# Performance work log

Hardware: AMD Instinct MI355X
Metric: run time of the kernel (lower is better)

## Reference

```python
import jax, jax.numpy as jnp
import numpy as np

N = 20000      # nodes
E = 160000     # edges (before self loops)
F = 256        # num_features
HID = 64       # hidden_channels
H = 4          # num_heads
HC = HID // H  # head channels = 16
C = 10         # num_classes
K = 3          # hops
ALPHA = 0.1
CST = 1e-5


def setup_inputs() -> dict:
    key = jax.random.key(0)
    ks = jax.random.split(key, 12)
    node_feat = jax.random.normal(ks[0], (N, F), dtype=jnp.float32)
    edge_index = jax.random.randint(ks[1], (2, E), 0, N, dtype=jnp.int32)

    def lin(k, fan_in, fan_out):
        b = 1.0 / np.sqrt(fan_in)
        kw, kb = jax.random.split(k)
        W = jax.random.uniform(kw, (fan_in, fan_out), jnp.float32, -b, b)
        bias = jax.random.uniform(kb, (fan_out,), jnp.float32, -b, b)
        return W, bias

    W_in, b_in = lin(ks[2], F, HID)
    Wq, bq = lin(ks[3], HID, H * HC)
    Wk, bk = lin(ks[4], HID, H * HC)
    Wv, bv = lin(ks[5], HID, H * C)
    W_out, b_out = lin(ks[6], H * C, C)

    # hopwise: alpha*(1-alpha)^k, last entry (1-alpha)^K
    hw = ALPHA * (1 - ALPHA) ** np.arange(K + 1, dtype=np.float32)
    hw[-1] = (1 - ALPHA) ** K
    hopwise = jnp.asarray(hw, dtype=jnp.float32)
    # temp: uniform one-head vector normalized by L1, tiled per head
    bound = np.sqrt(3.0 / (K + 1))
    onehead = jax.random.uniform(ks[7], (K + 1,), jnp.float32, -bound, bound)
    onehead = onehead / jnp.sum(jnp.abs(onehead))
    temp = jnp.tile(onehead[None, :], (H, 1))  # [H, K+1]

    return dict(node_feat=node_feat, edge_index=edge_index, W_in=W_in, b_in=b_in,
                Wq=Wq, bq=bq, Wk=Wk, bk=bk, Wv=Wv, bv=bv,
                W_out=W_out, b_out=b_out, hopwise=hopwise, temp=temp)


def reference(node_feat, edge_index, W_in, b_in, Wq, bq, Wk, bk, Wv, bv,
              W_out, b_out, hopwise, temp):
    # add self loops
    loops = jnp.arange(N, dtype=edge_index.dtype)
    ei = jnp.concatenate([edge_index, jnp.stack([loops, loops])], axis=1)
    row, col = ei[0], ei[1]
    # symmetric-normalized laplacian weights
    deg = jnp.zeros((N,), node_feat.dtype).at[col].add(1.0)
    dis = jnp.where(deg > 0, 1.0 / jnp.sqrt(jnp.maximum(deg, 1.0)), 0.0)
    norm = dis[row] * dis[col]  # [E+N]

    x = jax.nn.relu(node_feat @ W_in + b_in)                      # [N, HID]
    Q = (1.0 + jax.nn.elu(x @ Wq + bq)).reshape(N, H, HC)
    Kt = (1.0 + jax.nn.elu(x @ Wk + bk)).reshape(N, H, HC)
    V = (x @ Wv + bv).reshape(N, H, C)

    M = jnp.einsum('nhi,nhj->nhij', Kt, V)                        # [N, H, HC, C]
    hidden = V * hopwise[0]
    # NOTE: faithful to torch: softmax over dim=-2 of temp [H, K+1] == head axis
    layerwise = jax.nn.softmax(temp, axis=0)                      # [H, K+1]

    for hop in range(K):
        M = jax.ops.segment_sum(norm[:, None, None, None] * M[row], col, num_segments=N)
        Kt = jax.ops.segment_sum(norm[:, None, None] * Kt[row], col, num_segments=N)
        Hh = jnp.einsum('nhi,nhij->nhj', Q, M)                    # [N, H, C]
        Cd = jnp.einsum('nhi,nhi->nh', Q, Kt)[..., None] + CST    # [N, H, 1]
        gamma = hopwise[hop + 1] * layerwise[:, hop + 1][:, None]  # [H, 1]
        hidden = hidden + gamma * (Hh / Cd)

    out = hidden.reshape(N, H * C) @ W_out + b_out                # [N, C]
    return out
```

## Files before the change

### kernel.cpp

```cpp
#include <hip/hip_runtime.h>
#include <stdint.h>

#define kN   20000
#define kE   160000
#define kET  (kN + kE)
#define kF   256
#define kHID 64
#define kH   4
#define kHC  16
#define kC   10
#define kK   3
#define kCST 1e-5f
#define kBN  32

__device__ __forceinline__ uint16_t f2bf(float x) {
    uint32_t u = __float_as_uint(x);
    u += 0x7fffu + ((u >> 16) & 1u);
    return (uint16_t)(u >> 16);
}
__device__ __forceinline__ float lo16(uint32_t p) { return __uint_as_float(p << 16); }
__device__ __forceinline__ float hi16(uint32_t p) { return __uint_as_float(p & 0xffff0000u); }
__device__ __forceinline__ uint32_t pack2(float a, float b) {
    return ((uint32_t)f2bf(b) << 16) | (uint32_t)f2bf(a);
}

__global__ void deg_kernel(const int* __restrict__ ei, int* __restrict__ deg) {
    int e = blockIdx.x * blockDim.x + threadIdx.x;
    if (e >= kET) return;
    int c = (e < kE) ? ei[kE + e] : (e - kE);
    atomicAdd(&deg[c], 1);
}

__global__ __launch_bounds__(1024) void scan_kernel(
    const int* __restrict__ deg, int* __restrict__ ptr,
    const float* __restrict__ hopwise, const float* __restrict__ temp,
    float* __restrict__ gammas) {
    __shared__ int wsums[16];
    __shared__ int wexcl[16];
    const int CH = 20;
    int t = threadIdx.x;
    int base = t * CH;
    int s = 0;
    for (int i = 0; i < CH; ++i) {
        int idx = base + i;
        if (idx < kN) s += deg[idx];
    }
    int incl = s;
#pragma unroll
    for (int off = 1; off < 64; off <<= 1) {
        int v = __shfl_up(incl, off, 64);
        if ((t & 63) >= off) incl += v;
    }
    int wid = t >> 6;
    if ((t & 63) == 63) wsums[wid] = incl;
    __syncthreads();
    if (t < 16) {
        int p = 0;
        for (int j = 0; j < t; ++j) p += wsums[j];
        wexcl[t] = p;
    }
    __syncthreads();
    int running = wexcl[wid] + incl - s;
    for (int i = 0; i < CH; ++i) {
        int idx = base + i;
        if (idx < kN) { ptr[idx] = running; running += deg[idx]; }
    }
    if (base < kN && base + CH >= kN) ptr[kN] = running;
    if (t == 0) {
        for (int k = 1; k <= kK; ++k) {
            float mx = -1e30f;
            for (int h = 0; h < kH; ++h) mx = fmaxf(mx, temp[h * (kK + 1) + k]);
            float ex[kH]; float sum = 0.f;
            for (int h = 0; h < kH; ++h) { ex[h] = __expf(temp[h * (kK + 1) + k] - mx); sum += ex[h]; }
            for (int h = 0; h < kH; ++h) gammas[(k - 1) * kH + h] = hopwise[k] * ex[h] / sum;
        }
    }
}

__global__ void scatter_kernel(const int* __restrict__ ei, const int* __restrict__ deg,
                               const int* __restrict__ ptr, int* __restrict__ cursor,
                               int* __restrict__ src, float* __restrict__ wgt) {
    int e = blockIdx.x * blockDim.x + threadIdx.x;
    if (e >= kET) return;
    int r, c;
    if (e < kE) { r = ei[e]; c = ei[kE + e]; } else { r = c = e - kE; }
    float wv = rsqrtf((float)deg[r]) * rsqrtf((float)deg[c]);
    int pos = ptr[c] + atomicAdd(&cursor[c], 1);
    src[pos] = r;
    wgt[pos] = wv;
}

__global__ __launch_bounds__(256) void proj_kernel(
    const float* __restrict__ feat, const float* __restrict__ W_in, const float* __restrict__ b_in,
    const float* __restrict__ Wq, const float* __restrict__ bq,
    const float* __restrict__ Wk, const float* __restrict__ bk,
    const float* __restrict__ Wv, const float* __restrict__ bv,
    const float* __restrict__ hopwise,
    float* __restrict__ Qg, float* __restrict__ Ktg, float* __restrict__ hidden,
    float* __restrict__ Vg) {
    __shared__ float sF[kBN * 68];
    __shared__ float sW[64 * 68];
    __shared__ float sX[kBN * 68];

    int t = threadIdx.x;
    int tx = t & 15, ty = t >> 4;
    int n0 = blockIdx.x * kBN;
    int r0 = ty * 2, r1 = ty * 2 + 1;

    float acc[2][4];
#pragma unroll
    for (int i = 0; i < 2; ++i)
#pragma unroll
        for (int j = 0; j < 4; ++j) acc[i][j] = 0.f;

    for (int ks = 0; ks < 4; ++ks) {
        int k0 = ks * 64;
#pragma unroll
        for (int i = 0; i < 2; ++i) {
            int slot = t + 256 * i;
            int row = slot >> 4, cg = slot & 15;
            *(float4*)&sF[row * 68 + cg * 4] =
                *(const float4*)&feat[(size_t)(n0 + row) * kF + k0 + cg * 4];
        }
#pragma unroll
        for (int i = 0; i < 4; ++i) {
            int slot = t + 256 * i;
            int row = slot >> 4, cg = slot & 15;
            *(float4*)&sW[row * 68 + cg * 4] =
                *(const float4*)&W_in[(size_t)(k0 + row) * kHID + cg * 4];
        }
        __syncthreads();
#pragma unroll 8
        for (int kk = 0; kk < 64; ++kk) {
            float4 b = *(float4*)&sW[kk * 68 + tx * 4];
            float a0 = sF[r0 * 68 + kk], a1 = sF[r1 * 68 + kk];
            acc[0][0] += a0 * b.x; acc[0][1] += a0 * b.y;
            acc[0][2] += a0 * b.z; acc[0][3] += a0 * b.w;
            acc[1][0] += a1 * b.x; acc[1][1] += a1 * b.y;
            acc[1][2] += a1 * b.z; acc[1][3] += a1 * b.w;
        }
        __syncthreads();
    }
    {
        float bb[4];
#pragma unroll
        for (int j = 0; j < 4; ++j) bb[j] = b_in[tx * 4 + j];
#pragma unroll
        for (int i = 0; i < 2; ++i) {
            float4 xr;
            xr.x = fmaxf(acc[i][0] + bb[0], 0.f);
            xr.y = fmaxf(acc[i][1] + bb[1], 0.f);
            xr.z = fmaxf(acc[i][2] + bb[2], 0.f);
            xr.w = fmaxf(acc[i][3] + bb[3], 0.f);
            *(float4*)&sX[(r0 + i) * 68 + tx * 4] = xr;
        }
    }
#pragma unroll
    for (int i = 0; i < 4; ++i) {
        int slot = t + 256 * i;
        int row = slot >> 4, cg = slot & 15;
        *(float4*)&sW[row * 68 + cg * 4] = *(const float4*)&Wq[(size_t)row * kHID + cg * 4];
    }
    __syncthreads();

    float qa[2][4];
#pragma unroll
    for (int i = 0; i < 2; ++i)
#pragma unroll
        for (int j = 0; j < 4; ++j) qa[i][j] = 0.f;
#pragma unroll 8
    for (int kk = 0; kk < 64; ++kk) {
        float4 b = *(float4*)&sW[kk * 68 + tx * 4];
        float a0 = sX[r0 * 68 + kk], a1 = sX[r1 * 68 + kk];
        qa[0][0] += a0 * b.x; qa[0][1] += a0 * b.y;
        qa[0][2] += a0 * b.z; qa[0][3] += a0 * b.w;
        qa[1][0] += a1 * b.x; qa[1][1] += a1 * b.y;
        qa[1][2] += a1 * b.z; qa[1][3] += a1 * b.w;
    }
    {
        float bqv[4];
#pragma unroll
        for (int j = 0; j < 4; ++j) bqv[j] = bq[tx * 4 + j];
#pragma unroll
        for (int i = 0; i < 2; ++i) {
            float4 qv;
            float q0 = qa[i][0] + bqv[0], q1 = qa[i][1] + bqv[1];
            float q2 = qa[i][2] + bqv[2], q3 = qa[i][3] + bqv[3];
            qv.x = (q0 > 0.f) ? 1.f + q0 : __expf(q0);
            qv.y = (q1 > 0.f) ? 1.f + q1 : __expf(q1);
            qv.z = (q2 > 0.f) ? 1.f + q2 : __expf(q2);
            qv.w = (q3 > 0.f) ? 1.f + q3 : __expf(q3);
            *(float4*)&Qg[(size_t)(n0 + r0 + i) * kHID + tx * 4] = qv;
        }
    }
    __syncthreads();
#pragma unroll
    for (int i = 0; i < 4; ++i) {
        int slot = t + 256 * i;
        int row = slot >> 4, cg = slot & 15;
        *(float4*)&sW[row * 68 + cg * 4] = *(const float4*)&Wk[(size_t)row * kHID + cg * 4];
    }
    __syncthreads();

    float ka[2][4];
#pragma unroll
    for (int i = 0; i < 2; ++i)
#pragma unroll
        for (int j = 0; j < 4; ++j) ka[i][j] = 0.f;
#pragma unroll 8
    for (int kk = 0; kk < 64; ++kk) {
        float4 b = *(float4*)&sW[kk * 68 + tx * 4];
        float a0 = sX[r0 * 68 + kk], a1 = sX[r1 * 68 + kk];
        ka[0][0] += a0 * b.x; ka[0][1] += a0 * b.y;
        ka[0][2] += a0 * b.z; ka[0][3] += a0 * b.w;
        ka[1][0] += a1 * b.x; ka[1][1] += a1 * b.y;
        ka[1][2] += a1 * b.z; ka[1][3] += a1 * b.w;
    }
    {
        float bkv[4];
#pragma unroll
        for (int j = 0; j < 4; ++j) bkv[j] = bk[tx * 4 + j];
#pragma unroll
        for (int i = 0; i < 2; ++i) {
            float4 kv;
            float k0v = ka[i][0] + bkv[0], k1v = ka[i][1] + bkv[1];
            float k2v = ka[i][2] + bkv[2], k3v = ka[i][3] + bkv[3];
            kv.x = (k0v > 0.f) ? 1.f + k0v : __expf(k0v);
            kv.y = (k1v > 0.f) ? 1.f + k1v : __expf(k1v);
            kv.z = (k2v > 0.f) ? 1.f + k2v : __expf(k2v);
            kv.w = (k3v > 0.f) ? 1.f + k3v : __expf(k3v);
            *(float4*)&Ktg[(size_t)(n0 + r0 + i) * kHID + tx * 4] = kv;
        }
    }
    __syncthreads();
#pragma unroll
    for (int i = 0; i < 3; ++i) {
        int slot = t + 256 * i;
        if (slot < 640) {
            int row = slot / 10, cg = slot % 10;
            *(float4*)&sW[row * 44 + cg * 4] = *(const float4*)&Wv[(size_t)row * 40 + cg * 4];
        }
    }
    __syncthreads();

    if (t < 160) {
        int txv = t % 10, tyv = t / 10;
        int vr0 = tyv * 2;
        float va[2][4];
#pragma unroll
        for (int i = 0; i < 2; ++i)
#pragma unroll
            for (int j = 0; j < 4; ++j) va[i][j] = 0.f;
#pragma unroll 8
        for (int kk = 0; kk < 64; ++kk) {
            float4 b = *(float4*)&sW[kk * 44 + txv * 4];
            float a0 = sX[vr0 * 68 + kk], a1 = sX[(vr0 + 1) * 68 + kk];
            va[0][0] += a0 * b.x; va[0][1] += a0 * b.y;
            va[0][2] += a0 * b.z; va[0][3] += a0 * b.w;
            va[1][0] += a1 * b.x; va[1][1] += a1 * b.y;
            va[1][2] += a1 * b.z; va[1][3] += a1 * b.w;
        }
        float bvv[4];
#pragma unroll
        for (int j = 0; j < 4; ++j) bvv[j] = bv[txv * 4 + j];
        float hw0 = hopwise[0];
#pragma unroll
        for (int i = 0; i < 2; ++i) {
            int row = vr0 + i;
            float4 vr;
            vr.x = va[i][0] + bvv[0]; vr.y = va[i][1] + bvv[1];
            vr.z = va[i][2] + bvv[2]; vr.w = va[i][3] + bvv[3];
            *(float4*)&Vg[(size_t)(n0 + row) * 40 + txv * 4] = vr;
            float4 hr;
            hr.x = vr.x * hw0; hr.y = vr.y * hw0; hr.z = vr.z * hw0; hr.w = vr.w * hw0;
            *(float4*)&hidden[(size_t)(n0 + row) * 40 + txv * 4] = hr;
        }
    }
}

__global__ __launch_bounds__(256) void hop0_kernel(
    const int* __restrict__ ptr, const int* __restrict__ src, const float* __restrict__ wgt,
    const float* __restrict__ Ktin, const float* __restrict__ Vin,
    const float* __restrict__ Q,
    uint16_t* __restrict__ Mout, float* __restrict__ Ktout,
    float* __restrict__ hidden, const float* __restrict__ gammas) {
    __shared__ float Ml[4][640];
    __shared__ float Ktl[4][64];
    __shared__ float Ql[4][64];
    int w = threadIdx.x >> 6;
    int l = threadIdx.x & 63;
    int n = blockIdx.x * 4 + w;
    int beg = ptr[n], end = ptr[n + 1];

    Ql[w][l] = Q[(size_t)n * 64 + l];

    int offK[5], offV[5];
#pragma unroll
    for (int c = 0; c < 5; ++c) {
        int v = 2 * l + 128 * c;
        int h = v / 160, r = v - h * 160;
        int i = r / 10, j = r - i * 10;
        offK[c] = h * 16 + i;
        offV[c] = h * 10 + j;
    }
    int vidx = (l < 40) ? l : l - 40;

    float m[10];
#pragma unroll
    for (int i = 0; i < 10; ++i) m[i] = 0.f;
    float kacc = 0.f;

    auto edge = [&](float kv, float vv, float wv) {
#pragma unroll
        for (int c = 0; c < 5; ++c) {
            float kc = __shfl(kv, offK[c], 64);
            float v0 = __shfl(vv, offV[c], 64);
            float v1 = __shfl(vv, offV[c] + 1, 64);
            float kw = wv * kc;
            m[2 * c]     += kw * v0;
            m[2 * c + 1] += kw * v1;
        }
        kacc += wv * kv;
    };

    int e = beg;
    for (; e + 2 <= end; e += 2) {
        int s0 = src[e], s1 = src[e + 1];
        float w0 = wgt[e], w1 = wgt[e + 1];
        float ka = Ktin[(size_t)s0 * 64 + l];
        float va = Vin[(size_t)s0 * 40 + vidx];
        float kb = Ktin[(size_t)s1 * 64 + l];
        float vb = Vin[(size_t)s1 * 40 + vidx];
        edge(ka, va, w0);
        edge(kb, vb, w1);
    }
    if (e < end) {
        float ka = Ktin[(size_t)src[e] * 64 + l];
        float va = Vin[(size_t)src[e] * 40 + vidx];
        edge(ka, va, wgt[e]);
    }

    {
        uint32_t* orow = (uint32_t*)Mout + (size_t)n * 320 + l;
        orow[0]   = pack2(m[0], m[1]);
        orow[64]  = pack2(m[2], m[3]);
        orow[128] = pack2(m[4], m[5]);
        orow[192] = pack2(m[6], m[7]);
        orow[256] = pack2(m[8], m[9]);
        Ktout[(size_t)n * 64 + l] = kacc;
    }
    *(float2*)&Ml[w][2 * l]         = make_float2(m[0], m[1]);
    *(float2*)&Ml[w][2 * (l + 64)]  = make_float2(m[2], m[3]);
    *(float2*)&Ml[w][2 * (l + 128)] = make_float2(m[4], m[5]);
    *(float2*)&Ml[w][2 * (l + 192)] = make_float2(m[6], m[7]);
    *(float2*)&Ml[w][2 * (l + 256)] = make_float2(m[8], m[9]);
    Ktl[w][l] = kacc;
    __syncthreads();

    int tt = threadIdx.x;
    if (tt < 160) {
        int ww = tt / 40, o = tt % 40;
        int h = o / 10, j = o % 10;
        const float* q  = &Ql[ww][h * 16];
        const float* kk = &Ktl[ww][h * 16];
        const float* mm = &Ml[ww][h * 160 + j];
        float cd = kCST, hh = 0.f;
#pragma unroll
        for (int i = 0; i < 16; ++i) { cd += q[i] * kk[i]; hh += q[i] * mm[i * 10]; }
        int nn = blockIdx.x * 4 + ww;
        hidden[(size_t)nn * 40 + o] += gammas[h] * hh / cd;
    }
}

template<bool LAST>
__global__ __launch_bounds__(256) void hop2_kernel(
    const int* __restrict__ ptr, const int* __restrict__ src, const float* __restrict__ wgt,
    const uint16_t* __restrict__ Min, uint16_t* __restrict__ Mout,
    const float* __restrict__ Ktin, float* __restrict__ Ktout,
    const float* __restrict__ Q, float* __restrict__ hidden,
    const float* __restrict__ gammas,
    const float* __restrict__ W_out, const float* __restrict__ b_out,
    float* __restrict__ out) {
    __shared__ float Ml[4][640];
    __shared__ float Ktl[4][64];
    __shared__ float Ql[4][64];
    __shared__ float Hl[4][40];
    int w = threadIdx.x >> 6;
    int l = threadIdx.x & 63;
    int n = blockIdx.x * 4 + w;
    int beg = ptr[n], end = ptr[n + 1];
    const uint32_t* Mw = (const uint32_t*)Min;

    Ql[w][l] = Q[(size_t)n * 64 + l];

    float m0=0,m1=0,m2=0,m3=0,m4=0,m5=0,m6=0,m7=0,m8=0,m9=0;
    float kacc = 0.f;
    int e = beg;
    for (; e + 4 <= end; e += 4) {
        int s0 = src[e], s1 = src[e + 1], s2 = src[e + 2], s3 = src[e + 3];
        float w0 = wgt[e], w1 = wgt[e + 1], w2 = wgt[e + 2], w3 = wgt[e + 3];
        const uint32_t* p0 = Mw + (size_t)s0 * 320 + l;
        const uint32_t* p1 = Mw + (size_t)s1 * 320 + l;
        const uint32_t* p2 = Mw + (size_t)s2 * 320 + l;
        const uint32_t* p3 = Mw + (size_t)s3 * 320 + l;
        uint32_t a0 = p0[0], a1 = p0[64], a2 = p0[128], a3 = p0[192], a4 = p0[256];
        uint32_t b0 = p1[0], b1 = p1[64], b2 = p1[128], b3 = p1[192], b4 = p1[256];
        uint32_t c0 = p2[0], c1 = p2[64], c2 = p2[128], c3 = p2[192], c4 = p2[256];
        uint32_t d0 = p3[0], d1 = p3[64], d2 = p3[128], d3 = p3[192], d4 = p3[256];
        float ka = Ktin[(size_t)s0 * 64 + l], kb = Ktin[(size_t)s1 * 64 + l];
        float kc = Ktin[(size_t)s2 * 64 + l], kd = Ktin[(size_t)s3 * 64 + l];
        m0 += w0 * lo16(a0); m1 += w0 * hi16(a0);
        m2 += w0 * lo16(a1); m3 += w0 * hi16(a1);
        m4 += w0 * lo16(a2); m5 += w0 * hi16(a2);
        m6 += w0 * lo16(a3); m7 += w0 * hi16(a3);
        m8 += w0 * lo16(a4); m9 += w0 * hi16(a4);
        m0 += w1 * lo16(b0); m1 += w1 * hi16(b0);
        m2 += w1 * lo16(b1); m3 += w1 * hi16(b1);
        m4 += w1 * lo16(b2); m5 += w1 * hi16(b2);
        m6 += w1 * lo16(b3); m7 += w1 * hi16(b3);
        m8 += w1 * lo16(b4); m9 += w1 * hi16(b4);
        m0 += w2 * lo16(c0); m1 += w2 * hi16(c0);
        m2 += w2 * lo16(c1); m3 += w2 * hi16(c1);
        m4 += w2 * lo16(c2); m5 += w2 * hi16(c2);
        m6 += w2 * lo16(c3); m7 += w2 * hi16(c3);
        m8 += w2 * lo16(c4); m9 += w2 * hi16(c4);
        m0 += w3 * lo16(d0); m1 += w3 * hi16(d0);
        m2 += w3 * lo16(d1); m3 += w3 * hi16(d1);
        m4 += w3 * lo16(d2); m5 += w3 * hi16(d2);
        m6 += w3 * lo16(d3); m7 += w3 * hi16(d3);
        m8 += w3 * lo16(d4); m9 += w3 * hi16(d4);
        kacc += w0 * ka + w1 * kb + w2 * kc + w3 * kd;
    }
    for (; e + 2 <= end; e += 2) {
        int s0 = src[e], s1 = src[e + 1];
        float w0 = wgt[e], w1 = wgt[e + 1];
        const uint32_t* p0 = Mw + (size_t)s0 * 320 + l;
        const uint32_t* p1 = Mw + (size_t)s1 * 320 + l;
        uint32_t a0 = p0[0], a1 = p0[64], a2 = p0[128], a3 = p0[192], a4 = p0[256];
        uint32_t b0 = p1[0], b1 = p1[64], b2 = p1[128], b3 = p1[192], b4 = p1[256];
        float ka = Ktin[(size_t)s0 * 64 + l], kb = Ktin[(size_t)s1 * 64 + l];
        m0 += w0 * lo16(a0); m1 += w0 * hi16(a0);
        m2 += w0 * lo16(a1); m3 += w0 * hi16(a1);
        m4 += w0 * lo16(a2); m5 += w0 * hi16(a2);
        m6 += w0 * lo16(a3); m7 += w0 * hi16(a3);
        m8 += w0 * lo16(a4); m9 += w0 * hi16(a4);
        m0 += w1 * lo16(b0); m1 += w1 * hi16(b0);
        m2 += w1 * lo16(b1); m3 += w1 * hi16(b1);
        m4 += w1 * lo16(b2); m5 += w1 * hi16(b2);
        m6 += w1 * lo16(b3); m7 += w1 * hi16(b3);
        m8 += w1 * lo16(b4); m9 += w1 * hi16(b4);
        kacc += w0 * ka + w1 * kb;
    }
    if (e < end) {
        int s0 = src[e];
        float w0 = wgt[e];
        const uint32_t* p0 = Mw + (size_t)s0 * 320 + l;
        uint32_t a0 = p0[0], a1 = p0[64], a2 = p0[128], a3 = p0[192], a4 = p0[256];
        float ka = Ktin[(size_t)s0 * 64 + l];
        m0 += w0 * lo16(a0); m1 += w0 * hi16(a0);
        m2 += w0 * lo16(a1); m3 += w0 * hi16(a1);
        m4 += w0 * lo16(a2); m5 += w0 * hi16(a2);
        m6 += w0 * lo16(a3); m7 += w0 * hi16(a3);
        m8 += w0 * lo16(a4); m9 += w0 * hi16(a4);
        kacc += w0 * ka;
    }

    *(float2*)&Ml[w][2 * l]         = make_float2(m0, m1);
    *(float2*)&Ml[w][2 * (l + 64)]  = make_float2(m2, m3);
    *(float2*)&Ml[w][2 * (l + 128)] = make_float2(m4, m5);
    *(float2*)&Ml[w][2 * (l + 192)] = make_float2(m6, m7);
    *(float2*)&Ml[w][2 * (l + 256)] = make_float2(m8, m9);
    Ktl[w][l] = kacc;
    if constexpr (!LAST) {
        uint32_t* orow = (uint32_t*)Mout + (size_t)n * 320 + l;
        orow[0]   = pack2(m0, m1);
        orow[64]  = pack2(m2, m3);
        orow[128] = pack2(m4, m5);
        orow[192] = pack2(m6, m7);
        orow[256] = pack2(m8, m9);
        Ktout[(size_t)n * 64 + l] = kacc;
    }
    __syncthreads();

    int tt = threadIdx.x;
    if (tt < 160) {
        int ww = tt / 40, o = tt % 40;
        int h = o / 10, j = o % 10;
        const float* q  = &Ql[ww][h * 16];
        const float* kk = &Ktl[ww][h * 16];
        const float* mm = &Ml[ww][h * 160 + j];
        float cd = kCST, hh = 0.f;
#pragma unroll
        for (int i = 0; i < 16; ++i) { cd += q[i] * kk[i]; hh += q[i] * mm[i * 10]; }
        int nn = blockIdx.x * 4 + ww;
        float val = hidden[(size_t)nn * 40 + o] + gammas[h] * hh / cd;
        if constexpr (!LAST) hidden[(size_t)nn * 40 + o] = val;
        else Hl[ww][o] = val;
    }
    if constexpr (LAST) {
        __syncthreads();
        if (tt < 40) {
            int ww = tt / 10, c = tt % 10;
            float acc = b_out[c];
#pragma unroll
            for (int i = 0; i < 40; ++i) acc += Hl[ww][i] * W_out[i * 10 + c];
            out[(size_t)(blockIdx.x * 4 + ww) * 10 + c] = acc;
        }
    }
}

extern "C" void kernel_launch(void* const* d_in, const int* in_sizes, int n_in,
                              void* d_out, int out_size, void* d_ws, size_t ws_size,
                              hipStream_t stream) {
    const float* feat   = (const float*)d_in[0];
    const int*   ei     = (const int*)d_in[1];
    const float* W_in   = (const float*)d_in[2];
    const float* b_in   = (const float*)d_in[3];
    const float* Wq     = (const float*)d_in[4];
    const float* bq     = (const float*)d_in[5];
    const float* Wk     = (const float*)d_in[6];
    const float* bk     = (const float*)d_in[7];
    const float* Wv     = (const float*)d_in[8];
    const float* bv     = (const float*)d_in[9];
    const float* W_out  = (const float*)d_in[10];
    const float* b_out  = (const float*)d_in[11];
    const float* hopwise= (const float*)d_in[12];
    const float* temp   = (const float*)d_in[13];
    float* out = (float*)d_out;

    char* ws = (char*)d_ws;
    size_t off = 0;
    auto alloc = [&](size_t bytes) -> void* {
        void* p = ws + off;
        off += (bytes + 255) & ~(size_t)255;
        return p;
    };
    int*      deg    = (int*)alloc((size_t)kN * 4);
    int*      cursor = (int*)alloc((size_t)kN * 4);
    int*      ptr    = (int*)alloc((size_t)(kN + 1) * 4);
    int*      csrc   = (int*)alloc((size_t)kET * 4);
    float*    cwgt   = (float*)alloc((size_t)kET * 4);
    float*    Q      = (float*)alloc((size_t)kN * kHID * 4);
    float*    Kt0    = (float*)alloc((size_t)kN * kHID * 4);
    float*    Kt1    = (float*)alloc((size_t)kN * kHID * 4);
    float*    Vg     = (float*)alloc((size_t)kN * kH * kC * 4);
    float*    hidden = (float*)alloc((size_t)kN * kH * kC * 4);
    float*    gammas = (float*)alloc(64);
    uint16_t* M1     = (uint16_t*)alloc((size_t)kN * 640 * 2);
    uint16_t* M2     = (uint16_t*)alloc((size_t)kN * 640 * 2);
    (void)ws_size; (void)in_sizes; (void)n_in; (void)out_size;

    size_t deg_span = (size_t)((char*)cursor - (char*)deg) + (size_t)kN * 4;
    hipMemsetAsync(deg, 0, deg_span, stream);

    deg_kernel<<<(kET + 255) / 256, 256, 0, stream>>>(ei, deg);
    scan_kernel<<<1, 1024, 0, stream>>>(deg, ptr, hopwise, temp, gammas);
    scatter_kernel<<<(kET + 255) / 256, 256, 0, stream>>>(ei, deg, ptr, cursor, csrc, cwgt);
    proj_kernel<<<kN / kBN, 256, 0, stream>>>(feat, W_in, b_in, Wq, bq, Wk, bk, Wv, bv,
                                              hopwise, Q, Kt0, hidden, Vg);
    hop0_kernel<<<kN / 4, 256, 0, stream>>>(ptr, csrc, cwgt, Kt0, Vg, Q, M1, Kt1, hidden,
                                            gammas + 0);
    hop2_kernel<false><<<kN / 4, 256, 0, stream>>>(ptr, csrc, cwgt, M1, M2, Kt1, Kt0, Q, hidden,
                                                   gammas + 4, W_out, b_out, out);
    hop2_kernel<true><<<kN / 4, 256, 0, stream>>>(ptr, csrc, cwgt, M2, M1, Kt0, Kt1, Q, hidden,
                                                  gammas + 8, W_out, b_out, out);
}
```

Before: 206.0 us.

## Parallelize CSR row-pointer scan across blocks and cut shuffles in hop0

Replaces the single-block 1024-thread prefix scan of node degrees with a three-kernel scan: per-block sums, a small scan over block sums (which also computes gammas), and a per-block row-pointer write. In hop0, each lane now owns one K element and broadcasts V with 10 shuffles per edge instead of 15 shuffles of K and V. The edge loop is unrolled to 4 edges for more loads in flight. The M output keeps the same flattened layout, but each lane now writes 5 contiguous words, which changes store coalescing. The scan now costs two extra kernel launches.

```diff
diff --git a/kernel.cpp b/kernel.cpp
--- a/kernel.cpp
+++ b/kernel.cpp
@@ -12,6 +12,7 @@
 #define kK   3
 #define kCST 1e-5f
 #define kBN  32
+#define kNB  ((kN + 255) / 256)
 
 __device__ __forceinline__ uint16_t f2bf(float x) {
     uint32_t u = __float_as_uint(x);
@@ -31,41 +32,36 @@
     atomicAdd(&deg[c], 1);
 }
 
-__global__ __launch_bounds__(1024) void scan_kernel(
-    const int* __restrict__ deg, int* __restrict__ ptr,
+__global__ __launch_bounds__(256) void degsum_kernel(const int* __restrict__ deg,
+                                                     int* __restrict__ partial) {
+    __shared__ int sw[4];
+    int t = threadIdx.x;
+    int idx = blockIdx.x * 256 + t;
+    int v = (idx < kN) ? deg[idx] : 0;
+#pragma unroll
+    for (int off = 32; off >= 1; off >>= 1) v += __shfl_xor(v, off, 64);
+    if ((t & 63) == 0) sw[t >> 6] = v;
+    __syncthreads();
+    if (t == 0) partial[blockIdx.x] = sw[0] + sw[1] + sw[2] + sw[3];
+}
+
+__global__ __launch_bounds__(128) void midscan_kernel(
+    const int* __restrict__ partial, int* __restrict__ offsets,
     const float* __restrict__ hopwise, const float* __restrict__ temp,
     float* __restrict__ gammas) {
-    __shared__ int wsums[16];
-    __shared__ int wexcl[16];
-    const int CH = 20;
+    __shared__ int ws0;
     int t = threadIdx.x;
-    int base = t * CH;
-    int s = 0;
-    for (int i = 0; i < CH; ++i) {
-        int idx = base + i;
-        if (idx < kN) s += deg[idx];
-    }
-    int incl = s;
+    int v = (t < kNB) ? partial[t] : 0;
+    int incl = v;
 #pragma unroll
     for (int off = 1; off < 64; off <<= 1) {
-        int v = __shfl_up(incl, off, 64);
-        if ((t & 63) >= off) incl += v;
-    }
-    int wid = t >> 6;
-    if ((t & 63) == 63) wsums[wid] = incl;
-    __syncthreads();
-    if (t < 16) {
-        int p = 0;
-        for (int j = 0; j < t; ++j) p += wsums[j];
-        wexcl[t] = p;
-    }
-    __syncthreads();
-    int running = wexcl[wid] + incl - s;
-    for (int i = 0; i < CH; ++i) {
-        int idx = base + i;
-        if (idx < kN) { ptr[idx] = running; running += deg[idx]; }
-    }
-    if (base < kN && base + CH >= kN) ptr[kN] = running;
+        int u = __shfl_up(incl, off, 64);
+        if ((t & 63) >= off) incl += u;
+    }
+    if (t == 63) ws0 = incl;
+    __syncthreads();
+    int add = (t >= 64) ? ws0 : 0;
+    if (t < kNB) offsets[t] = add + incl - v;
     if (t == 0) {
         for (int k = 1; k <= kK; ++k) {
             float mx = -1e30f;
@@ -75,6 +71,29 @@
             for (int h = 0; h < kH; ++h) gammas[(k - 1) * kH + h] = hopwise[k] * ex[h] / sum;
         }
     }
+}
+
+__global__ __launch_bounds__(256) void ptrw_kernel(const int* __restrict__ deg,
+                                                   const int* __restrict__ offsets,
+                                                   int* __restrict__ ptr) {
+    __shared__ int sw[4];
+    int t = threadIdx.x;
+    int idx = blockIdx.x * 256 + t;
+    int v = (idx < kN) ? deg[idx] : 0;
+    int incl = v;
+#pragma unroll
+    for (int off = 1; off < 64; off <<= 1) {
+        int u = __shfl_up(incl, off, 64);
+        if ((t & 63) >= off) incl += u;
+    }
+    int wid = t >> 6;
+    if ((t & 63) == 63) sw[wid] = incl;
+    __syncthreads();
+    int wadd = 0;
+    for (int j = 0; j < 4; ++j) wadd += (j < wid) ? sw[j] : 0;
+    int excl = offsets[blockIdx.x] + wadd + incl - v;
+    if (idx < kN) ptr[idx] = excl;
+    if (idx == kN - 1) ptr[kN] = excl + v;
 }
 
 __global__ void scatter_kernel(const int* __restrict__ ei, const int* __restrict__ deg,
@@ -294,15 +313,7 @@
 
     Ql[w][l] = Q[(size_t)n * 64 + l];
 
-    int offK[5], offV[5];
-#pragma unroll
-    for (int c = 0; c < 5; ++c) {
-        int v = 2 * l + 128 * c;
-        int h = v / 160, r = v - h * 160;
-        int i = r / 10, j = r - i * 10;
-        offK[c] = h * 16 + i;
-        offV[c] = h * 10 + j;
-    }
+    int base_v = 10 * (l >> 4);
     int vidx = (l < 40) ? l : l - 40;
 
     float m[10];
@@ -310,50 +321,43 @@
     for (int i = 0; i < 10; ++i) m[i] = 0.f;
     float kacc = 0.f;
 
-    auto edge = [&](float kv, float vv, float wv) {
-#pragma unroll
-        for (int c = 0; c < 5; ++c) {
-            float kc = __shfl(kv, offK[c], 64);
-            float v0 = __shfl(vv, offV[c], 64);
-            float v1 = __shfl(vv, offV[c] + 1, 64);
-            float kw = wv * kc;
-            m[2 * c]     += kw * v0;
-            m[2 * c + 1] += kw * v1;
-        }
-        kacc += wv * kv;
+    auto edge = [&](float kl, float vv, float wv) {
+        float kw = wv * kl;
+        kacc += wv * kl;
+#pragma unroll
+        for (int c = 0; c < 10; ++c) {
+            float vc = __shfl(vv, base_v + c, 64);
+            m[c] += kw * vc;
+        }
     };
 
     int e = beg;
-    for (; e + 2 <= end; e += 2) {
-        int s0 = src[e], s1 = src[e + 1];
-        float w0 = wgt[e], w1 = wgt[e + 1];
-        float ka = Ktin[(size_t)s0 * 64 + l];
-        float va = Vin[(size_t)s0 * 40 + vidx];
-        float kb = Ktin[(size_t)s1 * 64 + l];
-        float vb = Vin[(size_t)s1 * 40 + vidx];
-        edge(ka, va, w0);
-        edge(kb, vb, w1);
-    }
-    if (e < end) {
-        float ka = Ktin[(size_t)src[e] * 64 + l];
-        float va = Vin[(size_t)src[e] * 40 + vidx];
-        edge(ka, va, wgt[e]);
+    for (; e + 4 <= end; e += 4) {
+        int s0 = src[e], s1 = src[e + 1], s2 = src[e + 2], s3 = src[e + 3];
+        float w0 = wgt[e], w1 = wgt[e + 1], w2 = wgt[e + 2], w3 = wgt[e + 3];
+        float ka = Ktin[(size_t)s0 * 64 + l], va = Vin[(size_t)s0 * 40 + vidx];
+        float kb = Ktin[(size_t)s1 * 64 + l], vb = Vin[(size_t)s1 * 40 + vidx];
+        float kc = Ktin[(size_t)s2 * 64 + l], vc = Vin[(size_t)s2 * 40 + vidx];
+        float kd = Ktin[(size_t)s3 * 64 + l], vd = Vin[(size_t)s3 * 40 + vidx];
+        edge(ka, va, w0); edge(kb, vb, w1); edge(kc, vc, w2); edge(kd, vd, w3);
+    }
+    for (; e < end; ++e) {
+        int s0 = src[e];
+        edge(Ktin[(size_t)s0 * 64 + l], Vin[(size_t)s0 * 40 + vidx], wgt[e]);
     }
 
     {
-        uint32_t* orow = (uint32_t*)Mout + (size_t)n * 320 + l;
-        orow[0]   = pack2(m[0], m[1]);
-        orow[64]  = pack2(m[2], m[3]);
-        orow[128] = pack2(m[4], m[5]);
-        orow[192] = pack2(m[6], m[7]);
-        orow[256] = pack2(m[8], m[9]);
+        uint32_t* orow = (uint32_t*)Mout + (size_t)n * 320 + 5 * l;
+        orow[0] = pack2(m[0], m[1]);
+        orow[1] = pack2(m[2], m[3]);
+        orow[2] = pack2(m[4], m[5]);
+        orow[3] = pack2(m[6], m[7]);
+        orow[4] = pack2(m[8], m[9]);
         Ktout[(size_t)n * 64 + l] = kacc;
     }
-    *(float2*)&Ml[w][2 * l]         = make_float2(m[0], m[1]);
-    *(float2*)&Ml[w][2 * (l + 64)]  = make_float2(m[2], m[3]);
-    *(float2*)&Ml[w][2 * (l + 128)] = make_float2(m[4], m[5]);
-    *(float2*)&Ml[w][2 * (l + 192)] = make_float2(m[6], m[7]);
-    *(float2*)&Ml[w][2 * (l + 256)] = make_float2(m[8], m[9]);
+#pragma unroll
+    for (int c = 0; c < 10; c += 2)
+        *(float2*)&Ml[w][10 * l + c] = make_float2(m[c], m[c + 1]);
     Ktl[w][l] = kacc;
     __syncthreads();
 
@@ -538,6 +542,8 @@
     int*      deg    = (int*)alloc((size_t)kN * 4);
     int*      cursor = (int*)alloc((size_t)kN * 4);
     int*      ptr    = (int*)alloc((size_t)(kN + 1) * 4);
+    int*      partial= (int*)alloc((size_t)kNB * 4);
+    int*      offs   = (int*)alloc((size_t)kNB * 4);
     int*      csrc   = (int*)alloc((size_t)kET * 4);
     float*    cwgt   = (float*)alloc((size_t)kET * 4);
     float*    Q      = (float*)alloc((size_t)kN * kHID * 4);
@@ -554,7 +560,9 @@
     hipMemsetAsync(deg, 0, deg_span, stream);
 
     deg_kernel<<<(kET + 255) / 256, 256, 0, stream>>>(ei, deg);
-    scan_kernel<<<1, 1024, 0, stream>>>(deg, ptr, hopwise, temp, gammas);
+    degsum_kernel<<<kNB, 256, 0, stream>>>(deg, partial);
+    midscan_kernel<<<1, 128, 0, stream>>>(partial, offs, hopwise, temp, gammas);
+    ptrw_kernel<<<kNB, 256, 0, stream>>>(deg, offs, ptr);
     scatter_kernel<<<(kET + 255) / 256, 256, 0, stream>>>(ei, deg, ptr, cursor, csrc, cwgt);
     proj_kernel<<<kN / kBN, 256, 0, stream>>>(feat, W_in, b_in, Wq, bq, Wk, bk, Wv, bv,
                                               hopwise, Q, Kt0, hidden, Vg);
```

New measurement: 176.7 us. 14.2% less time.
